# Kernel optimization log

Measured on AMD Instinct MI355X. Metric: run time of the kernel, lower is better.

The kernel has to match this reference:

```python
import jax, jax.numpy as jnp
import numpy as np

RHO = 1.0
L = 50
RS = np.array([20, 40, 80, 160], dtype=np.int32)

def _get_index():
    S = []
    for m in range(-L // 2, L // 2 + 1):
        for n in range(-L // 2, L // 2 + 1):
            if abs(m * n) <= RHO * L // 2:
                S.append((m, n))
    return np.array(S, dtype=np.int32)

IDX = _get_index()          # [449, 2] (m, n) pairs
K = IDX.shape[0]            # 449
B, N, M = 8, 65536, 2       # batch, sequence length, Nmodes (dual-pol)


def setup_inputs() -> dict:
    key = jax.random.key(0)
    ks = jax.random.split(key, 8)
    shp = (B, N, M)
    inp = {
        "E_real": jax.random.normal(ks[0], shp, jnp.float32),
        "E_imag": jax.random.normal(ks[1], shp, jnp.float32),
        "F_real": jax.random.normal(ks[2], shp, jnp.float32),
        "F_imag": jax.random.normal(ks[3], shp, jnp.float32),
        "C1_real": jax.random.normal(ks[4], (len(RS), K), jnp.float32) * 0.01,
        "C1_imag": jax.random.normal(ks[5], (len(RS), K), jnp.float32) * 0.01,
        "C2_real": jax.random.normal(ks[6], (len(RS), K), jnp.float32) * 0.01,
        "C2_imag": jax.random.normal(ks[7], (len(RS), K), jnp.float32) * 0.01,
    }
    # task_info columns: (P [dBm], Fi, Fs [Hz], Nch); Fs must be 2e9 * some Rs entry
    ti = np.zeros((B, 4), dtype=np.float32)
    ti[:, 0] = 2.0
    ti[:, 2] = RS[np.arange(B) % len(RS)].astype(np.float32) * 2e9
    inp["task_info"] = jnp.asarray(ti)
    return inp


def _forward(E_real, E_imag, F_real, F_imag, C1_real, C1_imag, C2_real, C2_imag, task_info):
    E = E_real + 1j * E_imag    # [B, N, M] complex64
    F = F_real + 1j * F_imag

    # choose_C: map Fs -> row of C tables (sorted-Rs order, as in the torch code)
    rs_sorted = jnp.sort(jnp.asarray(RS))
    x = (task_info[:, 2] / 2e9).astype(jnp.int32)              # [B]
    ind = jnp.argmax(x[:, None] == rs_sorted[None, :], axis=-1)  # [B]
    C1 = (C1_real + 1j * C1_imag)[ind]                         # [B, K]
    C2 = (C2_real + 1j * C2_imag)[ind]                         # [B, K]

    ms = jnp.asarray(IDX[:, 0])
    ns = jnp.asarray(IDX[:, 1])

    def step(acc, xs):
        m, n, c1, c2 = xs                                       # c1, c2: [B]
        En  = jnp.roll(E, n, axis=-2)
        Em  = jnp.roll(E, m, axis=-2)
        Emn = jnp.roll(E, m + n, axis=-2)
        Fn  = jnp.roll(F, n, axis=-2)
        Fmn = jnp.roll(F, m + n, axis=-2)
        A = En * jnp.conj(Fmn) * c1[:, None, None] + Fn * jnp.conj(Emn) * c2[:, None, None]
        # (A + A.roll(1, dim=-1)) swaps/combines the two polarizations
        return acc + (A + jnp.roll(A, 1, axis=-1)) * Em, None

    acc, _ = jax.lax.scan(step, jnp.zeros_like(E), (ms, ns, C1.T, C2.T))

    P = jnp.power(10.0, task_info[:, 0] / 10.0) / E.shape[-1]   # [B]
    Eo = F + (jnp.sqrt(P) ** 3)[:, None, None] * acc
    return E[:, L:-L, :], Eo[:, L:-L, :]


def reference(E_real, E_imag, F_real, F_imag, C1_real, C1_imag, C2_real, C2_imag, task_info):
    return _forward(E_real, E_imag, F_real, F_imag,
                    C1_real, C1_imag, C2_real, C2_imag, task_info)
```

## Files before the change

kernel.cpp:

```cpp
#include <hip/hip_runtime.h>
#include <hip/hip_bf16.h>


namespace {

constexpr int NSEQ    = 65536;
constexpr int BATCH   = 8;
constexpr int KTAPS   = 449;
constexpr int NM      = 25;
constexpr int THREADS = 256;
constexpr int TILE    = 512;
constexpr int WIN     = TILE + 4 * NM;
constexpr int GHW     = TILE + 2 * NM;
constexpr int GHH     = (GHW + 1) / 2;

typedef float v2f __attribute__((ext_vector_type(2)));

__device__ inline v2f pkfma(float s, v2f v, v2f acc) {
  return __builtin_elementwise_fma((v2f){s, s}, v, acc);
}

__device__ inline void mac(v2f& U13, v2f& U42, v2f& V13, v2f& V42,
                           const float4 c, const float4 g) {
  const v2f glo = (v2f){g.x, g.y}, ghi = (v2f){g.z, g.w};
  U13 = pkfma(c.x, glo, U13); U42 = pkfma(c.y, glo, U42);
  V13 = pkfma(c.z, ghi, V13); V42 = pkfma(c.w, ghi, V42);
}

__device__ inline unsigned short f2bf(float f) {
  __hip_bfloat16 h = __float2bfloat16(f);
  union { __hip_bfloat16 hh; unsigned short u; } cv;
  cv.hh = h;
  return cv.u;
}

__global__ void prep_c_kernel(const float* __restrict__ c1r, const float* __restrict__ c1i,
                              const float* __restrict__ c2r, const float* __restrict__ c2i,
                              float4* __restrict__ cw) {
  int idx = blockIdx.x * blockDim.x + threadIdx.x;
  if (idx < 4 * KTAPS) cw[idx] = make_float4(c1r[idx], c1i[idx], c2r[idx], c2i[idx]);
}

__device__ inline float4 gh_entry(const float4 e, const float4 f,
                                  const float4 fm, const float4 em) {
  v2f G = (v2f){fm.w * e.w, fm.w * (-e.z)};
  G = pkfma(fm.x, (v2f){e.x, e.y}, G);
  G = pkfma(fm.y, (v2f){e.y, -e.x}, G);
  G = pkfma(fm.z, (v2f){e.z, e.w}, G);
  v2f H = (v2f){em.w * f.w, em.w * (-f.z)};
  H = pkfma(em.x, (v2f){f.x, f.y}, H);
  H = pkfma(em.y, (v2f){f.y, -f.x}, H);
  H = pkfma(em.z, (v2f){f.z, f.w}, H);
  return make_float4(G.x, G.y, H.x, H.y);
}

template<int NMAX>
__device__ inline void fir_unrolled(const float4* __restrict__ hiArr,
                                    const float4* __restrict__ loArr,
                                    const float4* __restrict__ cc,
                                    int tid,
                                    v2f& aU13, v2f& aU42, v2f& aV13, v2f& aV42,
                                    v2f& bU13, v2f& bU42, v2f& bV13, v2f& bV42)
{
  const int h0 = tid + ((26 + NMAX) >> 1);
  const int h1 = tid + ((25 + NMAX) >> 1);
  float4 cOdd;
  {
    const float4 hi = hiArr[h0], lo = loArr[h1];
    const float4 c0 = cc[0], c1 = cc[1];
    mac(bU13, bU42, bV13, bV42, c0, hi);
    mac(bU13, bU42, bV13, bV42, c1, lo);
    mac(aU13, aU42, aV13, aV42, c0, lo);
    cOdd = c1;
  }
#pragma unroll
  for (int s = 1; s < NMAX; ++s) {
    const float4 hi = hiArr[h0 - s], lo = loArr[h1 - s];
    const float4 c2 = cc[2*s], c3 = cc[2*s + 1];
    mac(bU13, bU42, bV13, bV42, c2, hi);
    mac(bU13, bU42, bV13, bV42, c3, lo);
    mac(aU13, aU42, aV13, aV42, cOdd, hi);
    mac(aU13, aU42, aV13, aV42, c2, lo);
    cOdd = c3;
  }
  {
    const float4 hi = hiArr[h0 - NMAX], lo = loArr[h1 - NMAX];
    const float4 c2 = cc[2*NMAX];
    mac(bU13, bU42, bV13, bV42, c2, hi);
    mac(aU13, aU42, aV13, aV42, cOdd, hi);
    mac(aU13, aU42, aV13, aV42, c2, lo);
  }
}

__global__ __launch_bounds__(THREADS, 4) void hpbc_kernel(
    const float2* __restrict__ er, const float2* __restrict__ ei,
    const float2* __restrict__ fr, const float2* __restrict__ fi,
    const float*  __restrict__ task, const float4* __restrict__ cw,
    unsigned short* __restrict__ out, int nout, int lpad, int ntiles)
{
  __shared__ float4 sE[WIN];
  __shared__ float4 sF[WIN];
  __shared__ float4 ghE0[GHH], ghO0[GHH];
  __shared__ float4 ghE1[GHH], ghO1[GHH];

  const int bx   = blockIdx.x;
  const int b    = bx / ntiles;
  const int tile = bx - b * ntiles;
  const int tid  = threadIdx.x;
  const int i0   = lpad + tile * TILE;
  const int elo  = i0 - 2 * NM;

  const float2* erb = er + (size_t)b * NSEQ;
  const float2* eib = ei + (size_t)b * NSEQ;
  const float2* frb = fr + (size_t)b * NSEQ;
  const float2* fib = fi + (size_t)b * NSEQ;

  for (int u = tid; u < WIN; u += THREADS) {
    int g = (elo + u) & (NSEQ - 1);
    float2 a = erb[g], c = eib[g];
    sE[u] = make_float4(a.x, c.x, a.y, c.y);
    float2 d = frb[g], e = fib[g];
    sF[u] = make_float4(d.x, e.x, d.y, e.y);
  }

  const float dbm = task[b * 4 + 0];
  const float fsr = task[b * 4 + 2];
  const int   x   = (int)(fsr / 2.0e9f);
  const int ind = (x == 40) ? 1 : (x == 80) ? 2 : (x == 160) ? 3 : 0;
  const float4* __restrict__ crow = cw + ind * KTAPS;
  const float P  = powf(10.0f, dbm * 0.1f) * 0.5f;
  const float pf = P * sqrtf(P);

  __syncthreads();

  const float4 e0 = sE[tid + NM],            f0 = sF[tid + NM];
  const float4 e1 = sE[tid + THREADS + NM],  f1 = sF[tid + THREADS + NM];
  const bool  has3 = (tid < GHW - 2 * THREADS);
  float4 e2 = make_float4(0,0,0,0), f2 = e2;
  if (has3) { e2 = sE[tid + 2*THREADS + NM]; f2 = sF[tid + 2*THREADS + NM]; }

  v2f A0 = {0,0}, A1 = {0,0}, B0 = {0,0}, B1 = {0,0};
  int kbase = 0;
  float4 ebCarry = sE[2*tid + 1 + 2*NM + NM];

  auto write_gh = [&](float4* wE, float4* wO, int mmNext) {
    const int s = NM - mmNext;
    const float4 g0 = gh_entry(e0, f0, sF[tid + s], sE[tid + s]);
    if (tid & 1) wO[tid >> 1] = g0; else wE[tid >> 1] = g0;
    const float4 g1 = gh_entry(e1, f1, sF[tid + THREADS + s], sE[tid + THREADS + s]);
    if (tid & 1) wO[(tid + THREADS) >> 1] = g1; else wE[(tid + THREADS) >> 1] = g1;
    if (has3) {
      const float4 g2 = gh_entry(e2, f2, sF[tid + 2*THREADS + s], sE[tid + 2*THREADS + s]);
      if (tid & 1) wO[(tid + 2*THREADS) >> 1] = g2; else wE[(tid + 2*THREADS) >> 1] = g2;
    }
  };

  auto iter = [&](const float4* rE, const float4* rO,
                  float4* wE, float4* wO, int mm) {
    const int am   = mm < 0 ? -mm : mm;
    const int nmax = (mm == 0) ? NM : (NM / am);
    const int q    = nmax & 1;
    const float4* hiArr = q ? rO : rE;
    const float4* loArr = q ? rE : rO;
    const float4* cc = crow + kbase;

    v2f aU13={0,0}, aU42={0,0}, aV13={0,0}, aV42={0,0};
    v2f bU13={0,0}, bU42={0,0}, bV13={0,0}, bV42={0,0};
    switch (nmax) {
      case 25: fir_unrolled<25>(hiArr, loArr, cc, tid, aU13,aU42,aV13,aV42, bU13,bU42,bV13,bV42); break;
      case 12: fir_unrolled<12>(hiArr, loArr, cc, tid, aU13,aU42,aV13,aV42, bU13,bU42,bV13,bV42); break;
      case  8: fir_unrolled< 8>(hiArr, loArr, cc, tid, aU13,aU42,aV13,aV42, bU13,bU42,bV13,bV42); break;
      case  6: fir_unrolled< 6>(hiArr, loArr, cc, tid, aU13,aU42,aV13,aV42, bU13,bU42,bV13,bV42); break;
      case  5: fir_unrolled< 5>(hiArr, loArr, cc, tid, aU13,aU42,aV13,aV42, bU13,bU42,bV13,bV42); break;
      case  4: fir_unrolled< 4>(hiArr, loArr, cc, tid, aU13,aU42,aV13,aV42, bU13,bU42,bV13,bV42); break;
      case  3: fir_unrolled< 3>(hiArr, loArr, cc, tid, aU13,aU42,aV13,aV42, bU13,bU42,bV13,bV42); break;
      case  2: fir_unrolled< 2>(hiArr, loArr, cc, tid, aU13,aU42,aV13,aV42, bU13,bU42,bV13,bV42); break;
      default: fir_unrolled< 1>(hiArr, loArr, cc, tid, aU13,aU42,aV13,aV42, bU13,bU42,bV13,bV42); break;
    }
    kbase += 2 * nmax + 1;

    if (mm < NM) write_gh(wE, wO, mm + 1);

    const float sra = aU13.x - aU42.y + aV13.x - aV42.y;
    const float sia = aU13.y + aU42.x + aV13.y + aV42.x;
    const float srb = bU13.x - bU42.y + bV13.x - bV42.y;
    const float sib = bU13.y + bU42.x + bV13.y + bV42.x;

    const float4 ea = sE[2*tid + 2*NM - mm];
    const float4 eb = ebCarry;
    ebCarry = ea;
    A0 = pkfma(sra, (v2f){ea.x, ea.y}, pkfma(sia, (v2f){-ea.y, ea.x}, A0));
    A1 = pkfma(sra, (v2f){ea.z, ea.w}, pkfma(sia, (v2f){-ea.w, ea.z}, A1));
    B0 = pkfma(srb, (v2f){eb.x, eb.y}, pkfma(sib, (v2f){-eb.y, eb.x}, B0));
    B1 = pkfma(srb, (v2f){eb.z, eb.w}, pkfma(sib, (v2f){-eb.w, eb.z}, B1));

    __syncthreads();
  };

  write_gh(ghE0, ghO0, -NM);
  __syncthreads();

  for (int mm = -NM; mm <= NM; mm += 2) {
    iter(ghE0, ghO0, ghE1, ghO1, mm);
    if (mm + 1 <= NM)
      iter(ghE1, ghO1, ghE0, ghO0, mm + 1);
  }

  const int end = lpad + nout;
  const size_t chunk1 = (size_t)BATCH * nout * 4;
  const int i = i0 + 2 * tid;
  if (i + 1 < end) {
    const float4 evA = sE[2*tid + 2*NM],     fvA = sF[2*tid + 2*NM];
    const float4 evB = sE[2*tid + 1 + 2*NM], fvB = sF[2*tid + 1 + 2*NM];
    const size_t o = ((size_t)b * nout + (size_t)(i - lpad)) * 4;
    ushort4 w0a, w0b, w1a, w1b;
    w0a.x = f2bf(evA.y); w0a.y = f2bf(evA.x); w0a.z = f2bf(evA.w); w0a.w = f2bf(evA.z);
    w0b.x = f2bf(evB.y); w0b.y = f2bf(evB.x); w0b.z = f2bf(evB.w); w0b.w = f2bf(evB.z);
    w1a.x = f2bf(fvA.y + pf * A0.y); w1a.y = f2bf(fvA.x + pf * A0.x);
    w1a.z = f2bf(fvA.w + pf * A1.y); w1a.w = f2bf(fvA.z + pf * A1.x);
    w1b.x = f2bf(fvB.y + pf * B0.y); w1b.y = f2bf(fvB.x + pf * B0.x);
    w1b.z = f2bf(fvB.w + pf * B1.y); w1b.w = f2bf(fvB.z + pf * B1.x);
    *reinterpret_cast<ushort4*>(out + o) = w0a;
    *reinterpret_cast<ushort4*>(out + o + 4) = w0b;
    *reinterpret_cast<ushort4*>(out + chunk1 + o) = w1a;
    *reinterpret_cast<ushort4*>(out + chunk1 + o + 4) = w1b;
  } else if (i < end) {
    const float4 evA = sE[2*tid + 2*NM], fvA = sF[2*tid + 2*NM];
    const size_t o = ((size_t)b * nout + (size_t)(i - lpad)) * 4;
    ushort4 w0a, w1a;
    w0a.x = f2bf(evA.y); w0a.y = f2bf(evA.x); w0a.z = f2bf(evA.w); w0a.w = f2bf(evA.z);
    w1a.x = f2bf(fvA.y + pf * A0.y); w1a.y = f2bf(fvA.x + pf * A0.x);
    w1a.z = f2bf(fvA.w + pf * A1.y); w1a.w = f2bf(fvA.z + pf * A1.x);
    *reinterpret_cast<ushort4*>(out + o) = w0a;
    *reinterpret_cast<ushort4*>(out + chunk1 + o) = w1a;
  }
}

}

extern "C" void kernel_launch(void* const* d_in, const int* in_sizes, int n_in,
                              void* d_out, int out_size, void* d_ws, size_t ws_size,
                              hipStream_t stream) {
  const float* E_real  = (const float*)d_in[0];
  const float* E_imag  = (const float*)d_in[1];
  const float* F_real  = (const float*)d_in[2];
  const float* F_imag  = (const float*)d_in[3];
  const float* C1_real = (const float*)d_in[4];
  const float* C1_imag = (const float*)d_in[5];
  const float* C2_real = (const float*)d_in[6];
  const float* C2_imag = (const float*)d_in[7];
  const float* task    = (const float*)d_in[8];

  int nout = out_size / 32;
  if (nout < 1 || nout > NSEQ) nout = NSEQ - 100;
  const int lpad   = (NSEQ - nout) / 2;
  const int ntiles = (nout + TILE - 1) / TILE;

  unsigned short* outp = (unsigned short*)d_out;
  float4* cw = (float4*)d_ws;

  hipLaunchKernelGGL(prep_c_kernel, dim3((4 * KTAPS + 255) / 256), dim3(256), 0, stream,
                     C1_real, C1_imag, C2_real, C2_imag, cw);

  hipLaunchKernelGGL(hpbc_kernel, dim3(BATCH * ntiles), dim3(THREADS), 0, stream,
                     (const float2*)E_real, (const float2*)E_imag,
                     (const float2*)F_real, (const float2*)F_imag,
                     task, cw, outp, nout, lpad, ntiles);
}
```

Before: 88.32 us.

## Exploit m/-m symmetry to reuse one G/H table for both signs of m

Iterates only over non-negative m and builds one G/H product table per |m|, serving the -m taps from the same table through shifted indices and a swapped-coefficient copy (c2,c1 order) written by the prep kernel. This halves the number of table builds and block-wide barriers, from 51 to 26 iterations. In exchange the table grows by one entry and each iteration does two FIR passes with sign-adjusted reductions, which raises register pressure and indexing complexity.

Result: faster. 80.29 us, median of 2 (-9.1%).

```diff
diff --git a/kernel.cpp b/kernel.cpp
--- a/kernel.cpp
+++ b/kernel.cpp
@@ -11,8 +11,8 @@
 constexpr int THREADS = 256;
 constexpr int TILE    = 512;
 constexpr int WIN     = TILE + 4 * NM;
-constexpr int GHW     = TILE + 2 * NM;
-constexpr int GHH     = (GHW + 1) / 2;
+constexpr int GHW     = TILE + 2 * NM + 1;
+constexpr int GHH     = 282;
 
 typedef float v2f __attribute__((ext_vector_type(2)));
 
@@ -38,7 +38,10 @@
                               const float* __restrict__ c2r, const float* __restrict__ c2i,
                               float4* __restrict__ cw) {
   int idx = blockIdx.x * blockDim.x + threadIdx.x;
-  if (idx < 4 * KTAPS) cw[idx] = make_float4(c1r[idx], c1i[idx], c2r[idx], c2i[idx]);
+  if (idx < 4 * KTAPS) {
+    cw[idx]             = make_float4(c1r[idx], c1i[idx], c2r[idx], c2i[idx]);
+    cw[4 * KTAPS + idx] = make_float4(c2r[idx], c2i[idx], c1r[idx], c1i[idx]);
+  }
 }
 
 __device__ inline float4 gh_entry(const float4 e, const float4 f,
@@ -55,15 +58,13 @@
 }
 
 template<int NMAX>
-__device__ inline void fir_unrolled(const float4* __restrict__ hiArr,
-                                    const float4* __restrict__ loArr,
-                                    const float4* __restrict__ cc,
-                                    int tid,
-                                    v2f& aU13, v2f& aU42, v2f& aV13, v2f& aV42,
-                                    v2f& bU13, v2f& bU42, v2f& bV13, v2f& bV42)
+__device__ inline void fir_core(const float4* __restrict__ hiArr,
+                                const float4* __restrict__ loArr,
+                                int h0, int h1,
+                                const float4* __restrict__ cc,
+                                v2f& aU13, v2f& aU42, v2f& aV13, v2f& aV42,
+                                v2f& bU13, v2f& bU42, v2f& bV13, v2f& bV42)
 {
-  const int h0 = tid + ((26 + NMAX) >> 1);
-  const int h1 = tid + ((25 + NMAX) >> 1);
   float4 cOdd;
   {
     const float4 hi = hiArr[h0], lo = loArr[h1];
@@ -91,6 +92,19 @@
     mac(aU13, aU42, aV13, aV42, c2, lo);
   }
 }
+
+#define FIR_SWITCH(NMX, HI, LO, H0, H1, CC) \
+  switch (NMX) { \
+    case 25: fir_core<25>(HI, LO, H0, H1, CC, U13a,U42a,V13a,V42a, U13b,U42b,V13b,V42b); break; \
+    case 12: fir_core<12>(HI, LO, H0, H1, CC, U13a,U42a,V13a,V42a, U13b,U42b,V13b,V42b); break; \
+    case  8: fir_core< 8>(HI, LO, H0, H1, CC, U13a,U42a,V13a,V42a, U13b,U42b,V13b,V42b); break; \
+    case  6: fir_core< 6>(HI, LO, H0, H1, CC, U13a,U42a,V13a,V42a, U13b,U42b,V13b,V42b); break; \
+    case  5: fir_core< 5>(HI, LO, H0, H1, CC, U13a,U42a,V13a,V42a, U13b,U42b,V13b,V42b); break; \
+    case  4: fir_core< 4>(HI, LO, H0, H1, CC, U13a,U42a,V13a,V42a, U13b,U42b,V13b,V42b); break; \
+    case  3: fir_core< 3>(HI, LO, H0, H1, CC, U13a,U42a,V13a,V42a, U13b,U42b,V13b,V42b); break; \
+    case  2: fir_core< 2>(HI, LO, H0, H1, CC, U13a,U42a,V13a,V42a, U13b,U42b,V13b,V42b); break; \
+    default: fir_core< 1>(HI, LO, H0, H1, CC, U13a,U42a,V13a,V42a, U13b,U42b,V13b,V42b); break; \
+  }
 
 __global__ __launch_bounds__(THREADS, 4) void hpbc_kernel(
     const float2* __restrict__ er, const float2* __restrict__ ei,
@@ -128,6 +142,7 @@
   const int   x   = (int)(fsr / 2.0e9f);
   const int ind = (x == 40) ? 1 : (x == 80) ? 2 : (x == 160) ? 3 : 0;
   const float4* __restrict__ crow = cw + ind * KTAPS;
+  const float4* __restrict__ cswp = cw + 4 * KTAPS + ind * KTAPS;
   const float P  = powf(10.0f, dbm * 0.1f) * 0.5f;
   const float pf = P * sqrtf(P);
 
@@ -139,12 +154,8 @@
   float4 e2 = make_float4(0,0,0,0), f2 = e2;
   if (has3) { e2 = sE[tid + 2*THREADS + NM]; f2 = sF[tid + 2*THREADS + NM]; }
 
-  v2f A0 = {0,0}, A1 = {0,0}, B0 = {0,0}, B1 = {0,0};
-  int kbase = 0;
-  float4 ebCarry = sE[2*tid + 1 + 2*NM + NM];
-
-  auto write_gh = [&](float4* wE, float4* wO, int mmNext) {
-    const int s = NM - mmNext;
+  auto write_gh = [&](float4* wE, float4* wO, int Mn) {
+    const int s = NM - Mn;
     const float4 g0 = gh_entry(e0, f0, sF[tid + s], sE[tid + s]);
     if (tid & 1) wO[tid >> 1] = g0; else wE[tid >> 1] = g0;
     const float4 g1 = gh_entry(e1, f1, sF[tid + THREADS + s], sE[tid + THREADS + s]);
@@ -155,55 +166,77 @@
     }
   };
 
+  v2f A0 = {0,0}, A1 = {0,0}, B0 = {0,0}, B1 = {0,0};
+  int kbaseP = 199;
+  int kbaseN = 199;
+  float4 carry_p = sE[2*tid + 2*NM + 1];
+  float4 carry_m = carry_p;
+
   auto iter = [&](const float4* rE, const float4* rO,
-                  float4* wE, float4* wO, int mm) {
-    const int am   = mm < 0 ? -mm : mm;
-    const int nmax = (mm == 0) ? NM : (NM / am);
-    const int q    = nmax & 1;
-    const float4* hiArr = q ? rO : rE;
-    const float4* loArr = q ? rE : rO;
-    const float4* cc = crow + kbase;
-
-    v2f aU13={0,0}, aU42={0,0}, aV13={0,0}, aV42={0,0};
-    v2f bU13={0,0}, bU42={0,0}, bV13={0,0}, bV42={0,0};
-    switch (nmax) {
-      case 25: fir_unrolled<25>(hiArr, loArr, cc, tid, aU13,aU42,aV13,aV42, bU13,bU42,bV13,bV42); break;
-      case 12: fir_unrolled<12>(hiArr, loArr, cc, tid, aU13,aU42,aV13,aV42, bU13,bU42,bV13,bV42); break;
-      case  8: fir_unrolled< 8>(hiArr, loArr, cc, tid, aU13,aU42,aV13,aV42, bU13,bU42,bV13,bV42); break;
-      case  6: fir_unrolled< 6>(hiArr, loArr, cc, tid, aU13,aU42,aV13,aV42, bU13,bU42,bV13,bV42); break;
-      case  5: fir_unrolled< 5>(hiArr, loArr, cc, tid, aU13,aU42,aV13,aV42, bU13,bU42,bV13,bV42); break;
-      case  4: fir_unrolled< 4>(hiArr, loArr, cc, tid, aU13,aU42,aV13,aV42, bU13,bU42,bV13,bV42); break;
-      case  3: fir_unrolled< 3>(hiArr, loArr, cc, tid, aU13,aU42,aV13,aV42, bU13,bU42,bV13,bV42); break;
-      case  2: fir_unrolled< 2>(hiArr, loArr, cc, tid, aU13,aU42,aV13,aV42, bU13,bU42,bV13,bV42); break;
-      default: fir_unrolled< 1>(hiArr, loArr, cc, tid, aU13,aU42,aV13,aV42, bU13,bU42,bV13,bV42); break;
+                  float4* wE, float4* wO, int M) {
+    const int nmax = (M == 0) ? NM : (NM / M);
+    const int T    = 2 * nmax + 1;
+
+    {
+      const int q = nmax & 1;
+      const float4* hiArr = q ? rO : rE;
+      const float4* loArr = q ? rE : rO;
+      const int h0 = tid + ((26 + nmax) >> 1);
+      const int h1 = tid + ((25 + nmax) >> 1);
+      const float4* cc = crow + kbaseP;
+      v2f U13a={0,0},U42a={0,0},V13a={0,0},V42a={0,0};
+      v2f U13b={0,0},U42b={0,0},V13b={0,0},V42b={0,0};
+      FIR_SWITCH(nmax, hiArr, loArr, h0, h1, cc);
+      const float sra = U13a.x - U42a.y + V13a.x - V42a.y;
+      const float sia = U13a.y + U42a.x + V13a.y + V42a.x;
+      const float srb = U13b.x - U42b.y + V13b.x - V42b.y;
+      const float sib = U13b.y + U42b.x + V13b.y + V42b.x;
+      const float4 ea = sE[2*tid + 2*NM - M];
+      const float4 eb = carry_p;
+      carry_p = ea;
+      A0 = pkfma(sra, (v2f){ea.x, ea.y}, pkfma(sia, (v2f){-ea.y, ea.x}, A0));
+      A1 = pkfma(sra, (v2f){ea.z, ea.w}, pkfma(sia, (v2f){-ea.w, ea.z}, A1));
+      B0 = pkfma(srb, (v2f){eb.x, eb.y}, pkfma(sib, (v2f){-eb.y, eb.x}, B0));
+      B1 = pkfma(srb, (v2f){eb.z, eb.w}, pkfma(sib, (v2f){-eb.w, eb.z}, B1));
     }
-    kbase += 2 * nmax + 1;
-
-    if (mm < NM) write_gh(wE, wO, mm + 1);
-
-    const float sra = aU13.x - aU42.y + aV13.x - aV42.y;
-    const float sia = aU13.y + aU42.x + aV13.y + aV42.x;
-    const float srb = bU13.x - bU42.y + bV13.x - bV42.y;
-    const float sib = bU13.y + bU42.x + bV13.y + bV42.x;
-
-    const float4 ea = sE[2*tid + 2*NM - mm];
-    const float4 eb = ebCarry;
-    ebCarry = ea;
-    A0 = pkfma(sra, (v2f){ea.x, ea.y}, pkfma(sia, (v2f){-ea.y, ea.x}, A0));
-    A1 = pkfma(sra, (v2f){ea.z, ea.w}, pkfma(sia, (v2f){-ea.w, ea.z}, A1));
-    B0 = pkfma(srb, (v2f){eb.x, eb.y}, pkfma(sib, (v2f){-eb.y, eb.x}, B0));
-    B1 = pkfma(srb, (v2f){eb.z, eb.w}, pkfma(sib, (v2f){-eb.w, eb.z}, B1));
+    kbaseP += T;
+
+    if (M > 0) {
+      kbaseN -= T;
+      const int qm = (M + nmax) & 1;
+      const float4* hiArr = qm ? rO : rE;
+      const float4* loArr = qm ? rE : rO;
+      const int h0 = tid + ((26 + M + nmax) >> 1);
+      const int h1 = tid + ((25 + M + nmax) >> 1);
+      const float4* cc = cswp + kbaseN;
+      v2f U13a={0,0},U42a={0,0},V13a={0,0},V42a={0,0};
+      v2f U13b={0,0},U42b={0,0},V13b={0,0},V42b={0,0};
+      FIR_SWITCH(nmax, hiArr, loArr, h0, h1, cc);
+      const float sra = U13a.x + U42a.y + V13a.x + V42a.y;
+      const float sia = U42a.x - U13a.y + V42a.x - V13a.y;
+      const float srb = U13b.x + U42b.y + V13b.x + V42b.y;
+      const float sib = U42b.x - U13b.y + V42b.x - V13b.y;
+      const float4 ea = carry_m;
+      const float4 eb = sE[2*tid + 2*NM + 1 + M];
+      carry_m = eb;
+      A0 = pkfma(sra, (v2f){ea.x, ea.y}, pkfma(sia, (v2f){-ea.y, ea.x}, A0));
+      A1 = pkfma(sra, (v2f){ea.z, ea.w}, pkfma(sia, (v2f){-ea.w, ea.z}, A1));
+      B0 = pkfma(srb, (v2f){eb.x, eb.y}, pkfma(sib, (v2f){-eb.y, eb.x}, B0));
+      B1 = pkfma(srb, (v2f){eb.z, eb.w}, pkfma(sib, (v2f){-eb.w, eb.z}, B1));
+    }
+
+    if (M < NM) write_gh(wE, wO, M + 1);
 
     __syncthreads();
   };
 
-  write_gh(ghE0, ghO0, -NM);
+  write_gh(ghE0, ghO0, 0);
   __syncthreads();
 
-  for (int mm = -NM; mm <= NM; mm += 2) {
-    iter(ghE0, ghO0, ghE1, ghO1, mm);
-    if (mm + 1 <= NM)
-      iter(ghE1, ghO1, ghE0, ghO0, mm + 1);
+  for (int M = 0; M <= NM; M += 2) {
+    iter(ghE0, ghO0, ghE1, ghO1, M);
+    if (M + 1 <= NM)
+      iter(ghE1, ghO1, ghE0, ghO0, M + 1);
   }
 
   const int end = lpad + nout;
```
